# Kernel tuning notes

Measured on AMD Instinct MI355X. Metric: run time of the kernel, lower is better.

Reference implementation:

```python
import jax, jax.numpy as jnp
import numpy as np

INPUT, HIDDEN, OUTPUT = 512, 1024, 512

def setup_inputs() -> dict:
    key = jax.random.key(0)
    ks = jax.random.split(key, 7)
    B, T = 64, 1024
    s_ih = 1.0 / np.sqrt(HIDDEN)
    x = jax.random.normal(ks[0], (B, T, INPUT), dtype=jnp.float32)
    W_ih = jax.random.uniform(ks[1], (HIDDEN, INPUT), minval=-s_ih, maxval=s_ih, dtype=jnp.float32)
    W_hh = jax.random.uniform(ks[2], (HIDDEN, HIDDEN), minval=-s_ih, maxval=s_ih, dtype=jnp.float32)
    b_ih = jax.random.uniform(ks[3], (HIDDEN,), minval=-s_ih, maxval=s_ih, dtype=jnp.float32)
    b_hh = jax.random.uniform(ks[4], (HIDDEN,), minval=-s_ih, maxval=s_ih, dtype=jnp.float32)
    s_o = 1.0 / np.sqrt(HIDDEN)
    W_out = jax.random.uniform(ks[5], (OUTPUT, HIDDEN), minval=-s_o, maxval=s_o, dtype=jnp.float32)
    b_out = jax.random.uniform(ks[6], (OUTPUT,), minval=-s_o, maxval=s_o, dtype=jnp.float32)
    return {"x": x, "W_ih": W_ih, "W_hh": W_hh, "b_ih": b_ih, "b_hh": b_hh,
            "W_out": W_out, "b_out": b_out}

def reference(x, W_ih, W_hh, b_ih, b_hh, W_out, b_out):
    B = x.shape[0]
    # Precompute input projection for all timesteps: [B, T, H]
    xp = jnp.einsum('bti,hi->bth', x, W_ih) + b_ih + b_hh
    h0 = jnp.zeros((B, W_hh.shape[0]), dtype=x.dtype)

    def step(h, xp_t):
        h_new = jnp.tanh(xp_t + h @ W_hh.T)
        return h_new, h_new

    _, hs = jax.lax.scan(step, h0, jnp.swapaxes(xp, 0, 1))  # hs: [T, B, H]
    hs = jnp.swapaxes(hs, 0, 1)  # [B, T, H]
    # Per-step output head, batched over all timesteps
    return jnp.einsum('bth,oh->bto', hs, W_out) + b_out
```

## Files before the change

kernel.cpp:

```cpp
#include <hip/hip_runtime.h>

typedef __attribute__((ext_vector_type(8))) short s16x8;
typedef __attribute__((ext_vector_type(4))) float fx4;

static __device__ __forceinline__ unsigned short f2bf(float f){
  unsigned u = __float_as_uint(f);
  return (unsigned short)((u + 0x7fffu + ((u>>16)&1u)) >> 16);
}
static __device__ __forceinline__ float bf2f(unsigned short s){
  return __uint_as_float(((unsigned)s)<<16);
}
static __device__ __forceinline__ void ld2_llc(const void* p0, const void* p1,
                                               uint4* o0, uint4* o1){
  uint4 a, b;
  asm volatile("global_load_dwordx4 %0, %2, off sc0 sc1\n\t"
               "global_load_dwordx4 %1, %3, off sc0 sc1\n\t"
               "s_waitcnt vmcnt(0)"
               : "=&v"(a), "=&v"(b) : "v"(p0), "v"(p1) : "memory");
  *o0 = a; *o1 = b;
}

__global__ void k_cvt_wout(const float* __restrict__ w, unsigned short* __restrict__ o){
  int g = blockIdx.x*256 + threadIdx.x;
  int idx = g*4;
  float4 f = *(const float4*)(w + idx);
  unsigned u0 = (unsigned)f2bf(f.x) | ((unsigned)f2bf(f.y)<<16);
  unsigned u1 = (unsigned)f2bf(f.z) | ((unsigned)f2bf(f.w)<<16);
  *(uint2*)(o + idx) = make_uint2(u0, u1);
}

__global__ __launch_bounds__(256) void k_gemm_xp(
    const float* __restrict__ X, const float* __restrict__ Wih,
    const float* __restrict__ bih, const float* __restrict__ bhh,
    unsigned short* __restrict__ XP){
  __shared__ unsigned short As[128][40];
  __shared__ unsigned short Bs[128][40];
  const int bm = blockIdx.x, bn = blockIdx.y;
  const int tid = threadIdx.x, w = tid>>6, l = tid&63;
  const int wm = w>>1, wn = w&1;
  const int m0 = bm*128, n0 = bn*128;
  fx4 acc[4][4] = {};
  for (int kb = 0; kb < 512; kb += 32){
    #pragma unroll
    for (int q=0;q<4;q++){
      int f = tid + q*256;
      int row = f>>3, c4 = (f&7)*4;
      float4 v = *(const float4*)(X + (m0+row)*512 + kb + c4);
      unsigned u0 = (unsigned)f2bf(v.x) | ((unsigned)f2bf(v.y)<<16);
      unsigned u1 = (unsigned)f2bf(v.z) | ((unsigned)f2bf(v.w)<<16);
      *(uint2*)&As[row][c4] = make_uint2(u0,u1);
    }
    #pragma unroll
    for (int q=0;q<4;q++){
      int f = tid + q*256;
      int row = f>>3, c4 = (f&7)*4;
      float4 v = *(const float4*)(Wih + (n0+row)*512 + kb + c4);
      unsigned u0 = (unsigned)f2bf(v.x) | ((unsigned)f2bf(v.y)<<16);
      unsigned u1 = (unsigned)f2bf(v.z) | ((unsigned)f2bf(v.w)<<16);
      *(uint2*)&Bs[row][c4] = make_uint2(u0,u1);
    }
    __syncthreads();
    const int kbase = (l>>4)*8;
    s16x8 a[4], b[4];
    #pragma unroll
    for (int mt=0;mt<4;mt++) a[mt] = *(const s16x8*)&As[wm*64 + mt*16 + (l&15)][kbase];
    #pragma unroll
    for (int nt=0;nt<4;nt++) b[nt] = *(const s16x8*)&Bs[wn*64 + nt*16 + (l&15)][kbase];
    #pragma unroll
    for (int mt=0;mt<4;mt++)
      #pragma unroll
      for (int nt=0;nt<4;nt++)
        acc[mt][nt] = __builtin_amdgcn_mfma_f32_16x16x32_bf16(a[mt], b[nt], acc[mt][nt], 0,0,0);
    __syncthreads();
  }
  #pragma unroll
  for (int nt=0;nt<4;nt++){
    int n = n0 + wn*64 + nt*16 + (l&15);
    float bias = bih[n] + bhh[n];
    #pragma unroll
    for (int mt=0;mt<4;mt++){
      #pragma unroll
      for (int r=0;r<4;r++){
        int grow = m0 + wm*64 + mt*16 + (l>>4)*4 + r;
        int bb = grow >> 10, t = grow & 1023;
        XP[(t*64 + bb)*1024 + n] = f2bf(acc[mt][nt][r] + bias);
      }
    }
  }
}

__global__ __launch_bounds__(512) void k_rnn(
    const float* __restrict__ Whh, const unsigned short* __restrict__ XP,
    unsigned short* __restrict__ HS){
  __shared__ unsigned short hlds[8][1032];
  const int wg = blockIdx.x;
  const int gi = wg & 7;
  const int gj = wg >> 3;
  const int bi = gi*8, cj = gj*128;
  const int tid = threadIdx.x, w = tid>>6, l = tid&63;
  const int kbase = (l>>4)*8;

  const int col = cj + w*16 + (l&15);
  s16x8 wf[32];
  #pragma unroll
  for (int kk=0; kk<32; kk++){
    const float* p = Whh + col*1024 + kk*32 + kbase;
    float4 v0 = *(const float4*)p;
    float4 v1 = *(const float4*)(p+4);
    s16x8 s;
    s[0]=(short)f2bf(v0.x); s[1]=(short)f2bf(v0.y); s[2]=(short)f2bf(v0.z); s[3]=(short)f2bf(v0.w);
    s[4]=(short)f2bf(v1.x); s[5]=(short)f2bf(v1.y); s[6]=(short)f2bf(v1.z); s[7]=(short)f2bf(v1.w);
    wf[kk]=s;
  }

  const int ecol = cj + w*16 + (l&15);

  {
    int e = tid*2;
    int row = e>>7, c = e&127;
    unsigned short h0 = f2bf(tanhf(bf2f(XP[(bi+row)*1024 + cj + c])));
    unsigned short h1 = f2bf(tanhf(bf2f(XP[(bi+row)*1024 + cj + c + 1])));
    unsigned pk = (unsigned)h0 | ((unsigned)h1<<16);
    __hip_atomic_store((unsigned*)&HS[((bi+row)*1024 + 0)*1024 + cj + c], pk,
                       __ATOMIC_RELAXED, __HIP_MEMORY_SCOPE_AGENT);
  }

  for (int s=1; s<1024; ++s){
    float xv[4];
    if (l < 32){
      #pragma unroll
      for (int r=0;r<4;r++)
        xv[r] = bf2f(XP[(s*64 + bi + (l>>4)*4 + r)*1024 + ecol]);
    }
    {
      int row = tid>>6, c8 = (tid&63)*16;
      const unsigned short* rowp = HS + ((bi+row)*1024 + (s-1))*1024 + c8;
      uint4 v0, v1;
      for(;;){
        ld2_llc(rowp, rowp+8, &v0, &v1);
        unsigned bad = 0u;
        #pragma unroll
        for (int j=0;j<4;j++){
          unsigned u = ((unsigned*)&v0)[j];
          bad |= (unsigned)((u & 0xFFFFu) == 0xFFFFu) | (unsigned)(u >= 0xFFFF0000u);
        }
        #pragma unroll
        for (int j=0;j<4;j++){
          unsigned u = ((unsigned*)&v1)[j];
          bad |= (unsigned)((u & 0xFFFFu) == 0xFFFFu) | (unsigned)(u >= 0xFFFF0000u);
        }
        if (!bad) break;
      }
      *(uint4*)&hlds[row][c8]     = v0;
      *(uint4*)&hlds[row][c8 + 8] = v1;
    }
    __syncthreads();
    const int arow = (l&15)&7;
    fx4 ac0 = {0.f,0.f,0.f,0.f}, ac1 = ac0, ac2 = ac0, ac3 = ac0;
    #pragma unroll
    for (int kk=0;kk<32;kk+=4){
      s16x8 a0 = *(const s16x8*)&hlds[arow][(kk+0)*32 + kbase];
      s16x8 a1 = *(const s16x8*)&hlds[arow][(kk+1)*32 + kbase];
      s16x8 a2 = *(const s16x8*)&hlds[arow][(kk+2)*32 + kbase];
      s16x8 a3 = *(const s16x8*)&hlds[arow][(kk+3)*32 + kbase];
      ac0 = __builtin_amdgcn_mfma_f32_16x16x32_bf16(a0, wf[kk+0], ac0, 0,0,0);
      ac1 = __builtin_amdgcn_mfma_f32_16x16x32_bf16(a1, wf[kk+1], ac1, 0,0,0);
      ac2 = __builtin_amdgcn_mfma_f32_16x16x32_bf16(a2, wf[kk+2], ac2, 0,0,0);
      ac3 = __builtin_amdgcn_mfma_f32_16x16x32_bf16(a3, wf[kk+3], ac3, 0,0,0);
    }
    fx4 acc = (ac0+ac1)+(ac2+ac3);
    if (l < 32){
      #pragma unroll
      for (int r=0;r<4;r++){
        int row = (l>>4)*4 + r;
        unsigned short hv = f2bf(tanhf(acc[r] + xv[r]));
        __hip_atomic_store(&HS[((bi+row)*1024 + s)*1024 + ecol], hv,
                           __ATOMIC_RELAXED, __HIP_MEMORY_SCOPE_AGENT);
      }
    }
  }
}

__global__ __launch_bounds__(512) void k_gemm_out(
    const unsigned short* __restrict__ HS, const unsigned short* __restrict__ WoutB,
    const float* __restrict__ bout, float* __restrict__ OUT){
  __shared__ unsigned short As[128][40];
  __shared__ unsigned short Bs[512][40];
  const int m0 = blockIdx.x*128;
  const int tid = threadIdx.x, w = tid>>6, l = tid&63;
  const int wm = w>>2, wn = w&3;
  fx4 acc[4][8] = {};
  for (int kb = 0; kb < 1024; kb += 32){
    {
      int row = tid>>2, c8 = (tid&3)*8;
      *(uint4*)&As[row][c8] = *(const uint4*)(HS + (m0+row)*1024 + kb + c8);
    }
    #pragma unroll
    for (int q=0;q<4;q++){
      int f = tid + q*512;
      int row = f>>2, c8 = (f&3)*8;
      *(uint4*)&Bs[row][c8] = *(const uint4*)(WoutB + row*1024 + kb + c8);
    }
    __syncthreads();
    const int kbase = (l>>4)*8;
    s16x8 a[4], b[8];
    #pragma unroll
    for (int mt=0;mt<4;mt++) a[mt] = *(const s16x8*)&As[wm*64 + mt*16 + (l&15)][kbase];
    #pragma unroll
    for (int nt=0;nt<8;nt++) b[nt] = *(const s16x8*)&Bs[wn*128 + nt*16 + (l&15)][kbase];
    #pragma unroll
    for (int mt=0;mt<4;mt++)
      #pragma unroll
      for (int nt=0;nt<8;nt++)
        acc[mt][nt] = __builtin_amdgcn_mfma_f32_16x16x32_bf16(a[mt], b[nt], acc[mt][nt], 0,0,0);
    __syncthreads();
  }
  #pragma unroll
  for (int nt=0;nt<8;nt++){
    int n = wn*128 + nt*16 + (l&15);
    float bias = bout[n];
    #pragma unroll
    for (int mt=0;mt<4;mt++){
      #pragma unroll
      for (int r=0;r<4;r++){
        int row = m0 + wm*64 + mt*16 + (l>>4)*4 + r;
        OUT[row*512 + n] = acc[mt][nt][r] + bias;
      }
    }
  }
}

extern "C" void kernel_launch(void* const* d_in, const int* in_sizes, int n_in,
                              void* d_out, int out_size, void* d_ws, size_t ws_size,
                              hipStream_t stream){
  const float* x    = (const float*)d_in[0];
  const float* Wih  = (const float*)d_in[1];
  const float* Whh  = (const float*)d_in[2];
  const float* bih  = (const float*)d_in[3];
  const float* bhh  = (const float*)d_in[4];
  const float* Wout = (const float*)d_in[5];
  const float* bout = (const float*)d_in[6];

  const size_t XP_BYTES = 134217728ull;
  unsigned short* XP    = (unsigned short*)d_ws;
  unsigned short* WoutB = (unsigned short*)((char*)d_ws + XP_BYTES);
  unsigned short* HS    = (unsigned short*)d_out;
  float*          OUT   = (float*)d_out;

  k_cvt_wout<<<512, 256, 0, stream>>>(Wout, WoutB);
  dim3 g1(512, 8);
  k_gemm_xp<<<g1, 256, 0, stream>>>(x, Wih, bih, bhh, XP);
  hipMemsetAsync(HS, 0xFF, 134217728ull, stream);
  k_rnn<<<64, 512, 0, stream>>>(Whh, XP, HS);
  k_gemm_out<<<512, 512, 0, stream>>>(HS, WoutB, bout, OUT);
}
```

Before: 2.920 ms.

## Interleave two independent batch groups per RNN workgroup to hide step latency

Each RNN workgroup now processes two 8-row batch groups (A and B) alternately within each timestep, with separate LDS buffers, and the grid is halved from 64 to 32 workgroups. The aim is to overlap group B's compute with the cross-workgroup polling latency of group A (and vice versa), and to reduce the number of workgroups that must synchronise through global memory. In exchange each workgroup does twice the serial work per step and fewer CUs are used. The hazard is that the two halves are serialised by __syncthreads and the spin-wait loads, so the hoped-for overlap may be limited.

```diff
diff --git a/kernel.cpp b/kernel.cpp
--- a/kernel.cpp
+++ b/kernel.cpp
@@ -92,11 +92,12 @@
 __global__ __launch_bounds__(512) void k_rnn(
     const float* __restrict__ Whh, const unsigned short* __restrict__ XP,
     unsigned short* __restrict__ HS){
-  __shared__ unsigned short hlds[8][1032];
+  __shared__ unsigned short hldsA[8][1032];
+  __shared__ unsigned short hldsB[8][1032];
   const int wg = blockIdx.x;
-  const int gi = wg & 7;
-  const int gj = wg >> 3;
-  const int bi = gi*8, cj = gj*128;
+  const int gi = wg & 3;
+  const int gj = wg >> 2;
+  const int biA = gi*16, biB = gi*16 + 8, cj = gj*128;
   const int tid = threadIdx.x, w = tid>>6, l = tid&63;
   const int kbase = (l>>4)*8;
 
@@ -114,8 +115,11 @@
   }
 
   const int ecol = cj + w*16 + (l&15);
-
-  {
+  const int srow = tid>>6, sc8 = (tid&63)*16;
+
+  #pragma unroll
+  for (int half=0; half<2; ++half){
+    int bi = half ? biB : biA;
     int e = tid*2;
     int row = e>>7, c = e&127;
     unsigned short h0 = f2bf(tanhf(bf2f(XP[(bi+row)*1024 + cj + c])));
@@ -126,56 +130,110 @@
   }
 
   for (int s=1; s<1024; ++s){
-    float xv[4];
-    if (l < 32){
-      #pragma unroll
-      for (int r=0;r<4;r++)
-        xv[r] = bf2f(XP[(s*64 + bi + (l>>4)*4 + r)*1024 + ecol]);
-    }
     {
-      int row = tid>>6, c8 = (tid&63)*16;
-      const unsigned short* rowp = HS + ((bi+row)*1024 + (s-1))*1024 + c8;
-      uint4 v0, v1;
-      for(;;){
-        ld2_llc(rowp, rowp+8, &v0, &v1);
-        unsigned bad = 0u;
+      float xv[4];
+      if (l < 32){
         #pragma unroll
-        for (int j=0;j<4;j++){
-          unsigned u = ((unsigned*)&v0)[j];
-          bad |= (unsigned)((u & 0xFFFFu) == 0xFFFFu) | (unsigned)(u >= 0xFFFF0000u);
+        for (int r=0;r<4;r++)
+          xv[r] = bf2f(XP[(s*64 + biA + (l>>4)*4 + r)*1024 + ecol]);
+      }
+      {
+        const unsigned short* rowp = HS + ((biA+srow)*1024 + (s-1))*1024 + sc8;
+        uint4 v0, v1;
+        for(;;){
+          ld2_llc(rowp, rowp+8, &v0, &v1);
+          unsigned bad = 0u;
+          #pragma unroll
+          for (int j=0;j<4;j++){
+            unsigned u = ((unsigned*)&v0)[j];
+            bad |= (unsigned)((u & 0xFFFFu) == 0xFFFFu) | (unsigned)(u >= 0xFFFF0000u);
+          }
+          #pragma unroll
+          for (int j=0;j<4;j++){
+            unsigned u = ((unsigned*)&v1)[j];
+            bad |= (unsigned)((u & 0xFFFFu) == 0xFFFFu) | (unsigned)(u >= 0xFFFF0000u);
+          }
+          if (!bad) break;
         }
+        *(uint4*)&hldsA[srow][sc8]     = v0;
+        *(uint4*)&hldsA[srow][sc8 + 8] = v1;
+      }
+      __syncthreads();
+      const int arow = (l&15)&7;
+      fx4 ac0 = {0.f,0.f,0.f,0.f}, ac1 = ac0, ac2 = ac0, ac3 = ac0;
+      #pragma unroll
+      for (int kk=0;kk<32;kk+=4){
+        s16x8 a0 = *(const s16x8*)&hldsA[arow][(kk+0)*32 + kbase];
+        s16x8 a1 = *(const s16x8*)&hldsA[arow][(kk+1)*32 + kbase];
+        s16x8 a2 = *(const s16x8*)&hldsA[arow][(kk+2)*32 + kbase];
+        s16x8 a3 = *(const s16x8*)&hldsA[arow][(kk+3)*32 + kbase];
+        ac0 = __builtin_amdgcn_mfma_f32_16x16x32_bf16(a0, wf[kk+0], ac0, 0,0,0);
+        ac1 = __builtin_amdgcn_mfma_f32_16x16x32_bf16(a1, wf[kk+1], ac1, 0,0,0);
+        ac2 = __builtin_amdgcn_mfma_f32_16x16x32_bf16(a2, wf[kk+2], ac2, 0,0,0);
+        ac3 = __builtin_amdgcn_mfma_f32_16x16x32_bf16(a3, wf[kk+3], ac3, 0,0,0);
+      }
+      fx4 acc = (ac0+ac1)+(ac2+ac3);
+      if (l < 32){
         #pragma unroll
-        for (int j=0;j<4;j++){
-          unsigned u = ((unsigned*)&v1)[j];
-          bad |= (unsigned)((u & 0xFFFFu) == 0xFFFFu) | (unsigned)(u >= 0xFFFF0000u);
+        for (int r=0;r<4;r++){
+          int row = (l>>4)*4 + r;
+          unsigned short hv = f2bf(tanhf(acc[r] + xv[r]));
+          __hip_atomic_store(&HS[((biA+row)*1024 + s)*1024 + ecol], hv,
+                             __ATOMIC_RELAXED, __HIP_MEMORY_SCOPE_AGENT);
         }
-        if (!bad) break;
-      }
-      *(uint4*)&hlds[row][c8]     = v0;
-      *(uint4*)&hlds[row][c8 + 8] = v1;
-    }
-    __syncthreads();
-    const int arow = (l&15)&7;
-    fx4 ac0 = {0.f,0.f,0.f,0.f}, ac1 = ac0, ac2 = ac0, ac3 = ac0;
-    #pragma unroll
-    for (int kk=0;kk<32;kk+=4){
-      s16x8 a0 = *(const s16x8*)&hlds[arow][(kk+0)*32 + kbase];
-      s16x8 a1 = *(const s16x8*)&hlds[arow][(kk+1)*32 + kbase];
-      s16x8 a2 = *(const s16x8*)&hlds[arow][(kk+2)*32 + kbase];
-      s16x8 a3 = *(const s16x8*)&hlds[arow][(kk+3)*32 + kbase];
-      ac0 = __builtin_amdgcn_mfma_f32_16x16x32_bf16(a0, wf[kk+0], ac0, 0,0,0);
-      ac1 = __builtin_amdgcn_mfma_f32_16x16x32_bf16(a1, wf[kk+1], ac1, 0,0,0);
-      ac2 = __builtin_amdgcn_mfma_f32_16x16x32_bf16(a2, wf[kk+2], ac2, 0,0,0);
-      ac3 = __builtin_amdgcn_mfma_f32_16x16x32_bf16(a3, wf[kk+3], ac3, 0,0,0);
-    }
-    fx4 acc = (ac0+ac1)+(ac2+ac3);
-    if (l < 32){
-      #pragma unroll
-      for (int r=0;r<4;r++){
-        int row = (l>>4)*4 + r;
-        unsigned short hv = f2bf(tanhf(acc[r] + xv[r]));
-        __hip_atomic_store(&HS[((bi+row)*1024 + s)*1024 + ecol], hv,
-                           __ATOMIC_RELAXED, __HIP_MEMORY_SCOPE_AGENT);
+      }
+    }
+    {
+      float xv[4];
+      if (l < 32){
+        #pragma unroll
+        for (int r=0;r<4;r++)
+          xv[r] = bf2f(XP[(s*64 + biB + (l>>4)*4 + r)*1024 + ecol]);
+      }
+      {
+        const unsigned short* rowp = HS + ((biB+srow)*1024 + (s-1))*1024 + sc8;
+        uint4 v0, v1;
+        for(;;){
+          ld2_llc(rowp, rowp+8, &v0, &v1);
+          unsigned bad = 0u;
+          #pragma unroll
+          for (int j=0;j<4;j++){
+            unsigned u = ((unsigned*)&v0)[j];
+            bad |= (unsigned)((u & 0xFFFFu) == 0xFFFFu) | (unsigned)(u >= 0xFFFF0000u);
+          }
+          #pragma unroll
+          for (int j=0;j<4;j++){
+            unsigned u = ((unsigned*)&v1)[j];
+            bad |= (unsigned)((u & 0xFFFFu) == 0xFFFFu) | (unsigned)(u >= 0xFFFF0000u);
+          }
+          if (!bad) break;
+        }
+        *(uint4*)&hldsB[srow][sc8]     = v0;
+        *(uint4*)&hldsB[srow][sc8 + 8] = v1;
+      }
+      __syncthreads();
+      const int arow = (l&15)&7;
+      fx4 ac0 = {0.f,0.f,0.f,0.f}, ac1 = ac0, ac2 = ac0, ac3 = ac0;
+      #pragma unroll
+      for (int kk=0;kk<32;kk+=4){
+        s16x8 a0 = *(const s16x8*)&hldsB[arow][(kk+0)*32 + kbase];
+        s16x8 a1 = *(const s16x8*)&hldsB[arow][(kk+1)*32 + kbase];
+        s16x8 a2 = *(const s16x8*)&hldsB[arow][(kk+2)*32 + kbase];
+        s16x8 a3 = *(const s16x8*)&hldsB[arow][(kk+3)*32 + kbase];
+        ac0 = __builtin_amdgcn_mfma_f32_16x16x32_bf16(a0, wf[kk+0], ac0, 0,0,0);
+        ac1 = __builtin_amdgcn_mfma_f32_16x16x32_bf16(a1, wf[kk+1], ac1, 0,0,0);
+        ac2 = __builtin_amdgcn_mfma_f32_16x16x32_bf16(a2, wf[kk+2], ac2, 0,0,0);
+        ac3 = __builtin_amdgcn_mfma_f32_16x16x32_bf16(a3, wf[kk+3], ac3, 0,0,0);
+      }
+      fx4 acc = (ac0+ac1)+(ac2+ac3);
+      if (l < 32){
+        #pragma unroll
+        for (int r=0;r<4;r++){
+          int row = (l>>4)*4 + r;
+          unsigned short hv = f2bf(tanhf(acc[r] + xv[r]));
+          __hip_atomic_store(&HS[((biB+row)*1024 + s)*1024 + ecol], hv,
+                             __ATOMIC_RELAXED, __HIP_MEMORY_SCOPE_AGENT);
+        }
       }
     }
   }
@@ -251,6 +309,6 @@
   dim3 g1(512, 8);
   k_gemm_xp<<<g1, 256, 0, stream>>>(x, Wih, bih, bhh, XP);
   hipMemsetAsync(HS, 0xFF, 134217728ull, stream);
-  k_rnn<<<64, 512, 0, stream>>>(Whh, XP, HS);
+  k_rnn<<<32, 512, 0, stream>>>(Whh, XP, HS);
   k_gemm_out<<<512, 512, 0, stream>>>(HS, WoutB, bout, OUT);
 }
```

Result: slower. 5.367 ms (+83.8%).
